# Kernel optimization log

Hardware: AMD Instinct MI355X
Metric: run time of the kernel (lower is better)

The kernel has to match this reference:

```python
import jax, jax.numpy as jnp
import numpy as np

N_NODES = 100000
N_EDGES = 25000
NNZ = 800000
D_IN = 256
D_OUT = 256


def setup_inputs() -> dict:
    key = jax.random.key(0)
    k1, k2, k3, k4, k5, k6, k7 = jax.random.split(key, 7)
    return {
        "input": jax.random.normal(k1, (N_NODES, D_IN), dtype=jnp.float32),
        "V": jax.random.randint(k2, (NNZ,), 0, N_NODES, dtype=jnp.int32),
        "E": jax.random.randint(k3, (NNZ,), 0, N_EDGES, dtype=jnp.int32),
        "degV": jax.random.uniform(k4, (N_NODES, 1), dtype=jnp.float32),
        "degE": jax.random.uniform(k5, (N_EDGES, 1), dtype=jnp.float32),
        "weight": jax.random.normal(k6, (D_IN, D_OUT), dtype=jnp.float32) / np.sqrt(D_OUT),
        "bias": jax.random.normal(k7, (D_OUT,), dtype=jnp.float32) / np.sqrt(D_OUT),
    }


def reference(input, V, E, degV, degE, weight, bias):
    num_nodes = degV.shape[0]
    num_edges = degE.shape[0]
    # dense projection: [N, D_in] @ [D_in, D_out]
    X = input @ weight
    # vertex -> edge: gather per-incidence node feats, scatter-mean into edges
    Xve = X[V]  # [nnz, D_out]
    esum = jax.ops.segment_sum(Xve, E, num_segments=num_edges)
    ecnt = jax.ops.segment_sum(jnp.ones((E.shape[0], 1), X.dtype), E, num_segments=num_edges)
    Xe = esum / jnp.maximum(ecnt, 1.0)  # scatter mean
    Xe = Xe * degE  # edge degree scaling
    # edge -> vertex: gather edge feats, scatter-sum into nodes
    Xev = Xe[E]  # [nnz, D_out]
    Xv = jax.ops.segment_sum(Xev, V, num_segments=num_nodes)
    return Xv * degV + bias
```

## Files before the change

### kernel.cpp

```cpp
#include <hip/hip_runtime.h>
#include <stdint.h>

#define N_NODES 100000
#define N_EDGES 25000
#define NNZ_    800000
#define D       256
#define NTOT    (N_EDGES + N_NODES)
#define SB      1024
#define NBLK    ((NTOT + SB) / SB)
#define MP      25024

#define SHE   9
#define SHV   11
#define WKE   512
#define WKV   2048
#define NBKE  ((N_EDGES + WKE - 1) / WKE)
#define NBKV  ((N_NODES + WKV - 1) / WKV)
#define NB    (NBKE + NBKV)
#define CAP   24576

#define SC1B ((NNZ_ / 16 + 255) / 256)
#define WB 256
#define CB ((N_NODES * D / 8 + 255) / 256)

typedef short  short8   __attribute__((ext_vector_type(8)));
typedef float  f32x4    __attribute__((ext_vector_type(4)));
typedef ushort ushortx8 __attribute__((ext_vector_type(8)));
typedef ushort ushortx4 __attribute__((ext_vector_type(4)));

__device__ __forceinline__ ushort f2bf(float f) {
    uint32_t u = __float_as_uint(f);
    uint32_t r = u + 0x7fffu + ((u >> 16) & 1u);
    return (ushort)(r >> 16);
}
__device__ __forceinline__ float bf2f(ushort u) {
    return __uint_as_float(((uint32_t)u) << 16);
}


__global__ void __launch_bounds__(256) front_kernel(const int* __restrict__ V,
                                                    const int* __restrict__ E,
                                                    int* __restrict__ gcur,
                                                    int2* __restrict__ pairs,
                                                    const float* __restrict__ W,
                                                    ushort* __restrict__ WT,
                                                    const float* __restrict__ in,
                                                    ushort* __restrict__ Xbf) {
    __shared__ int cnt[NB], base[NB], lcur[NB];
    int b = blockIdx.x, t = threadIdx.x;
    if (b < SC1B) {
        for (int j = t; j < NB; j += 256) cnt[j] = 0;
        __syncthreads();
        int i0 = (b * 256 + t) * 16;
        bool act = i0 < NNZ_;
        if (act) {
#pragma unroll
            for (int c = 0; c < 16; c += 4) {
                int4 e = *reinterpret_cast<const int4*>(E + i0 + c);
                int4 v = *reinterpret_cast<const int4*>(V + i0 + c);
                atomicAdd(&cnt[e.x >> SHE], 1);
                atomicAdd(&cnt[e.y >> SHE], 1);
                atomicAdd(&cnt[e.z >> SHE], 1);
                atomicAdd(&cnt[e.w >> SHE], 1);
                atomicAdd(&cnt[NBKE + (v.x >> SHV)], 1);
                atomicAdd(&cnt[NBKE + (v.y >> SHV)], 1);
                atomicAdd(&cnt[NBKE + (v.z >> SHV)], 1);
                atomicAdd(&cnt[NBKE + (v.w >> SHV)], 1);
            }
        }
        __syncthreads();
        for (int j = t; j < NB; j += 256) {
            int c = cnt[j];
            base[j] = c ? atomicAdd(&gcur[j], c) : 0;
            lcur[j] = 0;
        }
        __syncthreads();
        if (act) {
#pragma unroll
            for (int c = 0; c < 16; c += 4) {
                int4 e = *reinterpret_cast<const int4*>(E + i0 + c);
                int4 v = *reinterpret_cast<const int4*>(V + i0 + c);
                int ev[4] = {e.x, e.y, e.z, e.w};
                int vv[4] = {v.x, v.y, v.z, v.w};
#pragma unroll
                for (int k = 0; k < 4; ++k) {
                    int b1 = ev[k] >> SHE;
                    int p1 = base[b1] + atomicAdd(&lcur[b1], 1);
                    if (p1 < CAP) pairs[(size_t)b1 * CAP + p1] = make_int2(ev[k], vv[k]);
                    int b2 = NBKE + (vv[k] >> SHV);
                    int p2 = base[b2] + atomicAdd(&lcur[b2], 1);
                    if (p2 < CAP) pairs[(size_t)b2 * CAP + p2] = make_int2(vv[k], ev[k]);
                }
            }
        }
    } else if (b < SC1B + WB) {
        int g = (b - SC1B) * 256 + t;
        int n = g >> 8, k = g & 255;
        WT[(size_t)n * 256 + k] = f2bf(W[(size_t)k * 256 + n]);
    } else {
        int i = (b - SC1B - WB) * 256 + t;
        if (i >= N_NODES * D / 8) return;
        const f32x4* p = reinterpret_cast<const f32x4*>(in) + (size_t)i * 2;
        f32x4 a = __builtin_nontemporal_load(p);
        f32x4 c = __builtin_nontemporal_load(p + 1);
        ushortx8 o;
        o[0] = f2bf(a[0]); o[1] = f2bf(a[1]); o[2] = f2bf(a[2]); o[3] = f2bf(a[3]);
        o[4] = f2bf(c[0]); o[5] = f2bf(c[1]); o[6] = f2bf(c[2]); o[7] = f2bf(c[3]);
        *(reinterpret_cast<ushortx8*>(Xbf) + i) = o;
    }
}


__global__ void __launch_bounds__(256) count2(const int2* __restrict__ pairs,
                                              const int* __restrict__ gcur,
                                              int* __restrict__ cntC) {
    __shared__ int hist[WKV];
    int b = blockIdx.x, t = threadIdx.x;
    bool eside = b < NBKE;
    int kb    = eside ? b * WKE : (b - NBKE) * WKV;
    int wk    = eside ? WKE : WKV;
    int nk    = eside ? min(WKE, N_EDGES - kb) : min(WKV, N_NODES - kb);
    int obase = eside ? kb : N_EDGES + kb;
    for (int j = t; j < wk; j += 256) hist[j] = 0;
    __syncthreads();
    int n = min(gcur[b], CAP);
    const int2* p = pairs + (size_t)b * CAP;
    for (int i = t; i < n; i += 256) {
        int2 pr = p[i];
        atomicAdd(&hist[pr.x - kb], 1);
    }
    __syncthreads();
    for (int j = t; j < nk; j += 256) cntC[obase + j] = hist[j];
}


__global__ void __launch_bounds__(256) scan_bsum(const int* __restrict__ in,
                                                 int* __restrict__ bsum, int n) {
    __shared__ int sh[256];
    int b = blockIdx.x, t = threadIdx.x;
    int base = b * SB + t * 4;
    int s = 0;
    if (base + 4 <= n) {
        int4 v = *reinterpret_cast<const int4*>(in + base);
        s = v.x + v.y + v.z + v.w;
    } else {
        for (int k = 0; k < 4; ++k)
            if (base + k < n) s += in[base + k];
    }
    sh[t] = s;
    __syncthreads();
    for (int off = 128; off > 0; off >>= 1) {
        if (t < off) sh[t] += sh[t + off];
        __syncthreads();
    }
    if (t == 0) bsum[b] = sh[0];
}

__global__ void __launch_bounds__(128) scan_boff(int* __restrict__ bsum, int nb) {
    __shared__ int sh[128];
    int t = threadIdx.x;
    int v = (t < nb) ? bsum[t] : 0;
    sh[t] = v;
    __syncthreads();
    for (int off = 1; off < 128; off <<= 1) {
        int u = (t >= off) ? sh[t - off] : 0;
        __syncthreads();
        sh[t] += u;
        __syncthreads();
    }
    if (t < nb) bsum[t] = sh[t] - v;
}

__global__ void __launch_bounds__(256) scan_write(const int* __restrict__ in,
                                                  const int* __restrict__ bsum,
                                                  int* __restrict__ off, int n) {
    __shared__ int sh[256];
    int b = blockIdx.x, t = threadIdx.x;
    int base = b * SB + t * 4;
    int v0 = 0, v1 = 0, v2 = 0, v3 = 0;
    if (base + 4 <= n) {
        int4 v = *reinterpret_cast<const int4*>(in + base);
        v0 = v.x; v1 = v.y; v2 = v.z; v3 = v.w;
    } else {
        if (base + 0 < n) v0 = in[base + 0];
        if (base + 1 < n) v1 = in[base + 1];
        if (base + 2 < n) v2 = in[base + 2];
        if (base + 3 < n) v3 = in[base + 3];
    }
    int s = v0 + v1 + v2 + v3;
    sh[t] = s;
    __syncthreads();
    for (int o = 1; o < 256; o <<= 1) {
        int u = (t >= o) ? sh[t - o] : 0;
        __syncthreads();
        sh[t] += u;
        __syncthreads();
    }
    int excl = bsum[b] + sh[t] - s;
    if (base + 0 <= n) off[base + 0] = excl; excl += v0;
    if (base + 1 <= n) off[base + 1] = excl; excl += v1;
    if (base + 2 <= n) off[base + 2] = excl; excl += v2;
    if (base + 3 <= n) off[base + 3] = excl;
}


__global__ void __launch_bounds__(256) fill3(const int2* __restrict__ pairs,
                                             const int* __restrict__ gcur,
                                             const int* __restrict__ offC,
                                             int* __restrict__ adjAll) {
    __shared__ int cur[WKV];
    int b = blockIdx.x, t = threadIdx.x;
    bool eside = b < NBKE;
    int kb    = eside ? b * WKE : (b - NBKE) * WKV;
    int nk    = eside ? min(WKE, N_EDGES - kb) : min(WKV, N_NODES - kb);
    int obase = eside ? kb : N_EDGES + kb;
    for (int j = t; j < nk; j += 256) cur[j] = offC[obase + j];
    __syncthreads();
    int n = min(gcur[b], CAP);
    const int2* p = pairs + (size_t)b * CAP;
    for (int i = t; i < n; i += 256) {
        int2 pr = p[i];
        int slot = atomicAdd(&cur[pr.x - kb], 1);
        adjAll[slot] = pr.y;
    }
}


__device__ __forceinline__ void gather_rows(const ushort* __restrict__ src,
                                            const int* __restrict__ adjAll,
                                            int b, int cnt, int half, int col8,
                                            float a[8], int lane) {
    for (int c0 = 0; c0 < cnt; c0 += 64) {
        int rem = cnt - c0;
        int li = c0 + min(lane, rem - 1);
        int myidx = adjAll[b + li];
        int lim = min(rem, 64);
        for (int j0 = 0; j0 < lim; j0 += 8) {
            int r0 = __shfl(myidx, j0 + 0 + half, 64);
            int r1 = __shfl(myidx, j0 + 2 + half, 64);
            int r2 = __shfl(myidx, j0 + 4 + half, 64);
            int r3 = __shfl(myidx, j0 + 6 + half, 64);
            ushortx8 x0 = *reinterpret_cast<const ushortx8*>(src + (size_t)r0 * D + col8);
            ushortx8 x1 = *reinterpret_cast<const ushortx8*>(src + (size_t)r1 * D + col8);
            ushortx8 x2 = *reinterpret_cast<const ushortx8*>(src + (size_t)r2 * D + col8);
            ushortx8 x3 = *reinterpret_cast<const ushortx8*>(src + (size_t)r3 * D + col8);
            if (j0 + 0 + half < lim) {
#pragma unroll
                for (int k = 0; k < 8; ++k) a[k] += bf2f(x0[k]);
            }
            if (j0 + 2 + half < lim) {
#pragma unroll
                for (int k = 0; k < 8; ++k) a[k] += bf2f(x1[k]);
            }
            if (j0 + 4 + half < lim) {
#pragma unroll
                for (int k = 0; k < 8; ++k) a[k] += bf2f(x2[k]);
            }
            if (j0 + 6 + half < lim) {
#pragma unroll
                for (int k = 0; k < 8; ++k) a[k] += bf2f(x3[k]);
            }
        }
    }
}


__global__ void edge_agg(const ushort* __restrict__ Xbf, const int* __restrict__ adjAll,
                         const int* __restrict__ offC, const float* __restrict__ degE,
                         ushort* __restrict__ Ye) {
    int gid = blockIdx.x * blockDim.x + threadIdx.x;
    int edge = gid >> 6;
    int lane = gid & 63;
    if (edge >= N_EDGES) return;
    int half = lane >> 5;
    int col8 = (lane & 31) * 8;
    int b = offC[edge], e = offC[edge + 1];
    int cnt = e - b;
    float a[8] = {0.f, 0.f, 0.f, 0.f, 0.f, 0.f, 0.f, 0.f};
    gather_rows(Xbf, adjAll, b, cnt, half, col8, a, lane);
#pragma unroll
    for (int k = 0; k < 8; ++k) a[k] += __shfl_xor(a[k], 32, 64);
    float s = degE[edge] / (float)(cnt > 1 ? cnt : 1);
    int k0 = half * 4;
    ushortx4 o;
    o[0] = f2bf(a[k0 + 0] * s); o[1] = f2bf(a[k0 + 1] * s);
    o[2] = f2bf(a[k0 + 2] * s); o[3] = f2bf(a[k0 + 3] * s);
    *reinterpret_cast<ushortx4*>(Ye + (size_t)edge * D + col8 + k0) = o;
}


__global__ void __launch_bounds__(256) gemm_mfma(const ushort* __restrict__ A,
                                                 const ushort* __restrict__ WT,
                                                 ushort* __restrict__ C, int M) {
    int wid  = threadIdx.x >> 6;
    int lane = threadIdx.x & 63;
    int row0 = blockIdx.x * 64 + wid * 16;
    int lr  = lane & 15;
    int lk8 = (lane >> 4) * 8;
    f32x4 acc[16];
#pragma unroll
    for (int t = 0; t < 16; ++t) acc[t] = (f32x4){0.f, 0.f, 0.f, 0.f};
    int arow = row0 + lr;
    if (arow >= M) arow = M - 1;
    const ushort* aptr = A + (size_t)arow * D;
#pragma unroll
    for (int k0 = 0; k0 < D; k0 += 32) {
        short8 af = *reinterpret_cast<const short8*>(aptr + k0 + lk8);
#pragma unroll
        for (int t = 0; t < 16; ++t) {
            short8 bf = *reinterpret_cast<const short8*>(
                WT + (size_t)(t * 16 + lr) * D + k0 + lk8);
            acc[t] = __builtin_amdgcn_mfma_f32_16x16x32_bf16(af, bf, acc[t], 0, 0, 0);
        }
    }
    int crow = row0 + (lane >> 4) * 4;
#pragma unroll
    for (int t = 0; t < 16; ++t) {
        int ccol = t * 16 + lr;
#pragma unroll
        for (int r = 0; r < 4; ++r) {
            int rr = crow + r;
            if (rr < M) C[(size_t)rr * D + ccol] = f2bf(acc[t][r]);
        }
    }
}


__global__ void node_agg(const ushort* __restrict__ Ze, const int* __restrict__ adjAll,
                         const int* __restrict__ offC, const float* __restrict__ degV,
                         const float* __restrict__ bias, float* __restrict__ out) {
    int gid = blockIdx.x * blockDim.x + threadIdx.x;
    int node = gid >> 6;
    int lane = gid & 63;
    if (node >= N_NODES) return;
    int half = lane >> 5;
    int col8 = (lane & 31) * 8;
    int b = offC[N_EDGES + node], e = offC[N_EDGES + node + 1];
    int cnt = e - b;
    float a[8] = {0.f, 0.f, 0.f, 0.f, 0.f, 0.f, 0.f, 0.f};
    gather_rows(Ze, adjAll, b, cnt, half, col8, a, lane);
#pragma unroll
    for (int k = 0; k < 8; ++k) a[k] += __shfl_xor(a[k], 32, 64);
    float dv = degV[node];
    int k0 = half * 4;
    int c = col8 + k0;
    f32x4 b4 = *reinterpret_cast<const f32x4*>(bias + c);
    f32x4 o;
    o[0] = a[k0 + 0] * dv + b4[0];
    o[1] = a[k0 + 1] * dv + b4[1];
    o[2] = a[k0 + 2] * dv + b4[2];
    o[3] = a[k0 + 3] * dv + b4[3];
    __builtin_nontemporal_store(o, reinterpret_cast<f32x4*>(out + (size_t)node * D + c));
}


extern "C" void kernel_launch(void* const* d_in, const int* in_sizes, int n_in,
                              void* d_out, int out_size, void* d_ws, size_t ws_size,
                              hipStream_t stream) {
    const float* input  = (const float*)d_in[0];
    const int*   V      = (const int*)d_in[1];
    const int*   E      = (const int*)d_in[2];
    const float* degV   = (const float*)d_in[3];
    const float* degE   = (const float*)d_in[4];
    const float* weight = (const float*)d_in[5];
    const float* bias   = (const float*)d_in[6];
    float* out = (float*)d_out;

    int* cntC   = (int*)d_ws;
    int* gcur   = cntC + NTOT;
    int* offC   = gcur + 128;
    int* bsum   = offC + (NTOT + 1);
    int* adjAll = bsum + 128;
    uintptr_t p = (uintptr_t)(adjAll + 2 * NNZ_);
    p = (p + 255) & ~(uintptr_t)255;
    ushort* Xbf = (ushort*)p;
    ushort* Ye  = Xbf + (size_t)N_NODES * D;
    ushort* Ze  = Ye + (size_t)MP * D;
    ushort* WT  = Ze + (size_t)MP * D;
    int2* pairs = (int2*)Ye;

    hipMemsetAsync(cntC, 0, (size_t)(NTOT + 128) * sizeof(int), stream);

    front_kernel<<<SC1B + WB + CB, 256, 0, stream>>>(V, E, gcur, pairs,
                                                     weight, WT, input, Xbf);

    count2<<<NB, 256, 0, stream>>>(pairs, gcur, cntC);
    scan_bsum<<<NBLK, 256, 0, stream>>>(cntC, bsum, NTOT);
    scan_boff<<<1, 128, 0, stream>>>(bsum, NBLK);
    scan_write<<<NBLK, 256, 0, stream>>>(cntC, bsum, offC, NTOT);
    fill3<<<NB, 256, 0, stream>>>(pairs, gcur, offC, adjAll);

    edge_agg<<<(N_EDGES * 64 + 255) / 256, 256, 0, stream>>>(Xbf, adjAll, offC, degE, Ye);

    gemm_mfma<<<MP / 64, 256, 0, stream>>>(Ye, WT, Ze, N_EDGES);

    node_agg<<<(N_NODES * 64 + 255) / 256, 256, 0, stream>>>(Ze, adjAll, offC, degV, bias, out);
}
```

Before: 251.3 us.

## Fuse CSR count, scan and fill into one per-bucket kernel

Replaces the five-kernel CSR build (count histogram, three-stage global scan, fill) with a single build_csr kernel. Each bucket block histograms its own pairs, computes its global base by summing the preceding buckets' pair counts from gcur, does a local scan in shared memory, writes offsets and fills adjacency. This removes four kernel launches, the cntC memset and the global count array round trips. In exchange, pairs are read twice within one block and each block does a serial prefix over earlier bucket counts. Correctness relies on bucket counts staying below CAP.

```diff
diff --git a/kernel.cpp b/kernel.cpp
--- a/kernel.cpp
+++ b/kernel.cpp
@@ -6,8 +6,6 @@
 #define NNZ_    800000
 #define D       256
 #define NTOT    (N_EDGES + N_NODES)
-#define SB      1024
-#define NBLK    ((NTOT + SB) / SB)
 #define MP      25024
 
 #define SHE   9
@@ -111,116 +109,63 @@
 }
 
 
-__global__ void __launch_bounds__(256) count2(const int2* __restrict__ pairs,
-                                              const int* __restrict__ gcur,
-                                              int* __restrict__ cntC) {
+__global__ void __launch_bounds__(256) build_csr(const int2* __restrict__ pairs,
+                                                 const int* __restrict__ gcur,
+                                                 int* __restrict__ offC,
+                                                 int* __restrict__ adjAll) {
     __shared__ int hist[WKV];
-    int b = blockIdx.x, t = threadIdx.x;
-    bool eside = b < NBKE;
-    int kb    = eside ? b * WKE : (b - NBKE) * WKV;
-    int wk    = eside ? WKE : WKV;
-    int nk    = eside ? min(WKE, N_EDGES - kb) : min(WKV, N_NODES - kb);
-    int obase = eside ? kb : N_EDGES + kb;
-    for (int j = t; j < wk; j += 256) hist[j] = 0;
-    __syncthreads();
-    int n = min(gcur[b], CAP);
-    const int2* p = pairs + (size_t)b * CAP;
-    for (int i = t; i < n; i += 256) {
-        int2 pr = p[i];
-        atomicAdd(&hist[pr.x - kb], 1);
-    }
-    __syncthreads();
-    for (int j = t; j < nk; j += 256) cntC[obase + j] = hist[j];
-}
-
-
-__global__ void __launch_bounds__(256) scan_bsum(const int* __restrict__ in,
-                                                 int* __restrict__ bsum, int n) {
-    __shared__ int sh[256];
-    int b = blockIdx.x, t = threadIdx.x;
-    int base = b * SB + t * 4;
-    int s = 0;
-    if (base + 4 <= n) {
-        int4 v = *reinterpret_cast<const int4*>(in + base);
-        s = v.x + v.y + v.z + v.w;
-    } else {
-        for (int k = 0; k < 4; ++k)
-            if (base + k < n) s += in[base + k];
-    }
-    sh[t] = s;
-    __syncthreads();
-    for (int off = 128; off > 0; off >>= 1) {
-        if (t < off) sh[t] += sh[t + off];
-        __syncthreads();
-    }
-    if (t == 0) bsum[b] = sh[0];
-}
-
-__global__ void __launch_bounds__(128) scan_boff(int* __restrict__ bsum, int nb) {
-    __shared__ int sh[128];
-    int t = threadIdx.x;
-    int v = (t < nb) ? bsum[t] : 0;
-    sh[t] = v;
-    __syncthreads();
-    for (int off = 1; off < 128; off <<= 1) {
-        int u = (t >= off) ? sh[t - off] : 0;
-        __syncthreads();
-        sh[t] += u;
-        __syncthreads();
-    }
-    if (t < nb) bsum[t] = sh[t] - v;
-}
-
-__global__ void __launch_bounds__(256) scan_write(const int* __restrict__ in,
-                                                  const int* __restrict__ bsum,
-                                                  int* __restrict__ off, int n) {
-    __shared__ int sh[256];
-    int b = blockIdx.x, t = threadIdx.x;
-    int base = b * SB + t * 4;
-    int v0 = 0, v1 = 0, v2 = 0, v3 = 0;
-    if (base + 4 <= n) {
-        int4 v = *reinterpret_cast<const int4*>(in + base);
-        v0 = v.x; v1 = v.y; v2 = v.z; v3 = v.w;
-    } else {
-        if (base + 0 < n) v0 = in[base + 0];
-        if (base + 1 < n) v1 = in[base + 1];
-        if (base + 2 < n) v2 = in[base + 2];
-        if (base + 3 < n) v3 = in[base + 3];
-    }
-    int s = v0 + v1 + v2 + v3;
-    sh[t] = s;
-    __syncthreads();
-    for (int o = 1; o < 256; o <<= 1) {
-        int u = (t >= o) ? sh[t - o] : 0;
-        __syncthreads();
-        sh[t] += u;
-        __syncthreads();
-    }
-    int excl = bsum[b] + sh[t] - s;
-    if (base + 0 <= n) off[base + 0] = excl; excl += v0;
-    if (base + 1 <= n) off[base + 1] = excl; excl += v1;
-    if (base + 2 <= n) off[base + 2] = excl; excl += v2;
-    if (base + 3 <= n) off[base + 3] = excl;
-}
-
-
-__global__ void __launch_bounds__(256) fill3(const int2* __restrict__ pairs,
-                                             const int* __restrict__ gcur,
-                                             const int* __restrict__ offC,
-                                             int* __restrict__ adjAll) {
-    __shared__ int cur[WKV];
+    __shared__ int tsum[256];
+    __shared__ int bsum_sh[NB];
+    __shared__ int bbase_sh;
     int b = blockIdx.x, t = threadIdx.x;
     bool eside = b < NBKE;
     int kb    = eside ? b * WKE : (b - NBKE) * WKV;
     int nk    = eside ? min(WKE, N_EDGES - kb) : min(WKV, N_NODES - kb);
     int obase = eside ? kb : N_EDGES + kb;
-    for (int j = t; j < nk; j += 256) cur[j] = offC[obase + j];
-    __syncthreads();
+    for (int j = t; j < WKV; j += 256) hist[j] = 0;
+    if (t < NB) bsum_sh[t] = gcur[t];
+    __syncthreads();
+    if (t == 0) {
+        int s = 0;
+        for (int j = 0; j < b; ++j) s += bsum_sh[j];
+        bbase_sh = s;
+    }
     int n = min(gcur[b], CAP);
     const int2* p = pairs + (size_t)b * CAP;
     for (int i = t; i < n; i += 256) {
+        atomicAdd(&hist[p[i].x - kb], 1);
+    }
+    __syncthreads();
+    int bbase = bbase_sh;
+    int j0 = t * 8;
+    int s = 0;
+#pragma unroll
+    for (int j = 0; j < 8; ++j) s += hist[j0 + j];
+    tsum[t] = s;
+    __syncthreads();
+    for (int o = 1; o < 256; o <<= 1) {
+        int u = (t >= o) ? tsum[t - o] : 0;
+        __syncthreads();
+        tsum[t] += u;
+        __syncthreads();
+    }
+    int excl = tsum[t] - s;
+    int curv[8];
+#pragma unroll
+    for (int j = 0; j < 8; ++j) {
+        int h = hist[j0 + j];
+        curv[j] = bbase + excl;
+        if (j0 + j < nk) offC[obase + j0 + j] = bbase + excl;
+        excl += h;
+    }
+    __syncthreads();
+#pragma unroll
+    for (int j = 0; j < 8; ++j) hist[j0 + j] = curv[j];
+    if (b == NB - 1 && t == 0) offC[NTOT] = bbase + n;
+    __syncthreads();
+    for (int i = t; i < n; i += 256) {
         int2 pr = p[i];
-        int slot = atomicAdd(&cur[pr.x - kb], 1);
+        int slot = atomicAdd(&hist[pr.x - kb], 1);
         adjAll[slot] = pr.y;
     }
 }
@@ -366,11 +311,9 @@
     const float* bias   = (const float*)d_in[6];
     float* out = (float*)d_out;
 
-    int* cntC   = (int*)d_ws;
-    int* gcur   = cntC + NTOT;
+    int* gcur   = (int*)d_ws;
     int* offC   = gcur + 128;
-    int* bsum   = offC + (NTOT + 1);
-    int* adjAll = bsum + 128;
+    int* adjAll = offC + (NTOT + 1);
     uintptr_t p = (uintptr_t)(adjAll + 2 * NNZ_);
     p = (p + 255) & ~(uintptr_t)255;
     ushort* Xbf = (ushort*)p;
@@ -379,16 +322,12 @@
     ushort* WT  = Ze + (size_t)MP * D;
     int2* pairs = (int2*)Ye;
 
-    hipMemsetAsync(cntC, 0, (size_t)(NTOT + 128) * sizeof(int), stream);
+    hipMemsetAsync(gcur, 0, 128 * sizeof(int), stream);
 
     front_kernel<<<SC1B + WB + CB, 256, 0, stream>>>(V, E, gcur, pairs,
                                                      weight, WT, input, Xbf);
 
-    count2<<<NB, 256, 0, stream>>>(pairs, gcur, cntC);
-    scan_bsum<<<NBLK, 256, 0, stream>>>(cntC, bsum, NTOT);
-    scan_boff<<<1, 128, 0, stream>>>(bsum, NBLK);
-    scan_write<<<NBLK, 256, 0, stream>>>(cntC, bsum, offC, NTOT);
-    fill3<<<NB, 256, 0, stream>>>(pairs, gcur, offC, adjAll);
+    build_csr<<<NB, 256, 0, stream>>>(pairs, gcur, offC, adjAll);
 
     edge_agg<<<(N_EDGES * 64 + 255) / 256, 256, 0, stream>>>(Xbf, adjAll, offC, degE, Ye);
 
```

After: 241.1 us. 4.1% less time.
